# Performance work log

Measured on AMD Instinct MI355X. Metric: run time of the kernel, lower is better.

## Reference

```python
import jax, jax.numpy as jnp
import numpy as np

N = 100000
E = 1600000
D_IN = 128
HEADS = 4
C = 16  # hidden // heads
NEG_SLOPE = 0.2


def setup_inputs() -> dict:
    key = jax.random.key(0)
    ks = jax.random.split(key, 8)
    x = jax.random.normal(ks[0], (N, D_IN), dtype=jnp.float32)
    edge_index = jax.random.randint(ks[1], (2, E), 0, N, dtype=jnp.int32)
    s = 1.0 / np.sqrt(D_IN)
    W_l = jax.random.normal(ks[2], (D_IN, HEADS * C), dtype=jnp.float32) * s
    b_l = jnp.zeros((HEADS * C,), dtype=jnp.float32)
    W_r = jax.random.normal(ks[3], (D_IN, HEADS * C), dtype=jnp.float32) * s
    b_r = jnp.zeros((HEADS * C,), dtype=jnp.float32)
    att = jax.random.normal(ks[4], (HEADS, C), dtype=jnp.float32) * (1.0 / np.sqrt(C))
    bias = jnp.zeros((HEADS * C,), dtype=jnp.float32)
    W_head = jax.random.normal(ks[5], (HEADS * C, 1), dtype=jnp.float32) * (1.0 / np.sqrt(HEADS * C))
    b_head = jnp.zeros((1,), dtype=jnp.float32)
    return {"x": x, "edge_index": edge_index, "W_l": W_l, "b_l": b_l,
            "W_r": W_r, "b_r": b_r, "att": att, "bias": bias,
            "W_head": W_head, "b_head": b_head}


def reference(x, edge_index, W_l, b_l, W_r, b_r, att, bias, W_head, b_head):
    # GATv2Conv (PyG semantics, add_self_loops=True, concat=True)
    n = x.shape[0]
    # add self loops
    loops = jnp.arange(n, dtype=edge_index.dtype)
    src = jnp.concatenate([edge_index[0], loops])  # source j
    dst = jnp.concatenate([edge_index[1], loops])  # target i
    # per-node linear projections -> [N, H, C]
    x_l = (x @ W_l + b_l).reshape(n, HEADS, C)
    x_r = (x @ W_r + b_r).reshape(n, HEADS, C)
    # per-edge attention logits: att . LeakyReLU(x_l[j] + x_r[i])
    e = x_l[src] + x_r[dst]                               # [E', H, C]
    e = jnp.where(e >= 0, e, NEG_SLOPE * e)
    logits = jnp.einsum('ehc,hc->eh', e, att)             # [E', H]
    # segment softmax over incoming edges of each target node
    seg_max = jax.ops.segment_max(logits, dst, num_segments=n)  # [N, H]
    expw = jnp.exp(logits - seg_max[dst])
    seg_sum = jax.ops.segment_sum(expw, dst, num_segments=n)
    alpha = expw / seg_sum[dst]                           # [E', H]
    # weighted scatter-aggregate of source messages
    msg = alpha[:, :, None] * x_l[src]                    # [E', H, C]
    out = jax.ops.segment_sum(msg, dst, num_segments=n)   # [N, H, C]
    out = out.reshape(n, HEADS * C) + bias
    # ReLU + Linear head
    h = jax.nn.relu(out)
    return (h @ W_head + b_head).squeeze(-1)              # [N]
```

## Files before the change

### kernel.cpp

```cpp
#include <hip/hip_runtime.h>
#include <hip/hip_bf16.h>
#include <hip/hip_fp16.h>

#define HC 64
#define D_IN 128
#define NEG_SLOPE 0.2f
#define BK 64
#define BCAP2 1536
#define NBIN 2048
#define L2E 1.44269504f

using f32x4 = __attribute__((ext_vector_type(4))) float;
using f16x8 = __attribute__((ext_vector_type(8))) _Float16;
using f16x2 = __attribute__((ext_vector_type(2))) _Float16;

__global__ void k_iota(int* __restrict__ p, int n) {
    int i = blockIdx.x * blockDim.x + threadIdx.x;
    if (i < n) p[i] = i * BCAP2;
}

__global__ __launch_bounds__(256, 3) void k_proj(
    const float* __restrict__ x,
    const float* __restrict__ Wl, const float* __restrict__ bl,
    const float* __restrict__ Wr, const float* __restrict__ br,
    __half* __restrict__ xlh, float* __restrict__ xr, int N) {
    __shared__ _Float16 sWT[128 * 136];
    __shared__ _Float16 sX[32 * 136];
    const int t = threadIdx.x;
    for (int idx = t; idx < 8192; idx += 256) {
        const int k = idx >> 6;
        const int c = idx & 63;
        sWT[c * 136 + k]        = (_Float16)Wl[idx];
        sWT[(c + 64) * 136 + k] = (_Float16)Wr[idx];
    }
    const int lane = t & 63;
    const int wave = t >> 6;
    const int m = lane & 15;
    const int q = lane >> 4;
    float bfu[2];
#pragma unroll
    for (int cc = 0; cc < 2; ++cc) {
        const int ct = wave * 2 + cc;
        const int ch = (ct & 3) * 16 + m;
        bfu[cc] = (ct < 4) ? bl[ch] : br[ch];
    }
    __syncthreads();

    const int ntrip = N >> 5;
    for (int trip = blockIdx.x; trip < ntrip; trip += gridDim.x) {
        const int i0 = trip << 5;
        for (int c = t; c < 1024; c += 256) {
            const int r = c >> 5, c4 = c & 31;
            float4 v = ((const float4*)(x + (size_t)(i0 + r) * D_IN))[c4];
            _Float16* dp = &sX[r * 136 + c4 * 4];
            dp[0] = (_Float16)v.x; dp[1] = (_Float16)v.y;
            dp[2] = (_Float16)v.z; dp[3] = (_Float16)v.w;
        }
        __syncthreads();
        f16x8 af[2][4];
#pragma unroll
        for (int tt = 0; tt < 2; ++tt)
#pragma unroll
            for (int kk = 0; kk < 4; ++kk)
                af[tt][kk] = *(const f16x8*)&sX[(tt * 16 + m) * 136 + kk * 32 + q * 8];
#pragma unroll
        for (int cc = 0; cc < 2; ++cc) {
            const int ct = wave * 2 + cc;
            const _Float16* bp = &sWT[(ct * 16 + m) * 136 + q * 8];
            f32x4 acc0 = {0.f, 0.f, 0.f, 0.f};
            f32x4 acc1 = {0.f, 0.f, 0.f, 0.f};
#pragma unroll
            for (int kk = 0; kk < 4; ++kk) {
                f16x8 bf = *(const f16x8*)(bp + kk * 32);
                acc0 = __builtin_amdgcn_mfma_f32_16x16x32_f16(af[0][kk], bf, acc0, 0, 0, 0);
                acc1 = __builtin_amdgcn_mfma_f32_16x16x32_f16(af[1][kk], bf, acc1, 0, 0, 0);
            }
            const float bv = bfu[cc];
            if (ct < 4) {
                const int ch = ct * 16 + m;
#pragma unroll
                for (int r = 0; r < 4; ++r) {
                    xlh[(size_t)(i0 + q * 4 + r) * HC + ch]      = __float2half(acc0[r] + bv);
                    xlh[(size_t)(i0 + 16 + q * 4 + r) * HC + ch] = __float2half(acc1[r] + bv);
                }
            } else {
                const int ch = (ct - 4) * 16 + m;
#pragma unroll
                for (int r = 0; r < 4; ++r) {
                    xr[(size_t)(i0 + q * 4 + r) * HC + ch]      = acc0[r] + bv;
                    xr[(size_t)(i0 + 16 + q * 4 + r) * HC + ch] = acc1[r] + bv;
                }
            }
        }
        __syncthreads();
    }
}

__global__ __launch_bounds__(256) void k_scat1(const int* __restrict__ src,
                                               const int* __restrict__ dst, int E,
                                               int* __restrict__ bfill,
                                               unsigned* __restrict__ coarse) {
    __shared__ int h[NBIN], bl[NBIN], cur[NBIN];
    const int t = threadIdx.x;
    for (int i = t; i < NBIN; i += 256) { h[i] = 0; cur[i] = 0; }
    __syncthreads();
    const int beg = blockIdx.x * 4096;
    int4 d4[4], s4[4];
#pragma unroll
    for (int r = 0; r < 4; ++r) {
        const int idx = beg + 4 * t + r * 1024;
        if (idx < E) {
            d4[r] = *(const int4*)(dst + idx);
            s4[r] = *(const int4*)(src + idx);
        } else { d4[r] = make_int4(-1, -1, -1, -1); }
    }
#pragma unroll
    for (int r = 0; r < 4; ++r) {
        if (d4[r].x >= 0) {
            atomicAdd(&h[d4[r].x >> 6], 1);
            atomicAdd(&h[d4[r].y >> 6], 1);
            atomicAdd(&h[d4[r].z >> 6], 1);
            atomicAdd(&h[d4[r].w >> 6], 1);
        }
    }
    __syncthreads();
    for (int i = t; i < NBIN; i += 256)
        bl[i] = h[i] ? atomicAdd(&bfill[i], h[i]) : 0;
    __syncthreads();
#pragma unroll
    for (int r = 0; r < 4; ++r) {
        if (d4[r].x >= 0) {
            const int dd[4] = {d4[r].x, d4[r].y, d4[r].z, d4[r].w};
            const int ss[4] = {s4[r].x, s4[r].y, s4[r].z, s4[r].w};
#pragma unroll
            for (int j = 0; j < 4; ++j) {
                const int bin = dd[j] >> 6;
                const int pos = atomicAdd(&cur[bin], 1);
                coarse[bl[bin] + pos] = ((unsigned)ss[j] << 6) | (unsigned)(dd[j] & 63);
            }
        }
    }
}

__device__ __forceinline__ float redpair(float v) {
    int a = __builtin_amdgcn_update_dpp(0, __float_as_int(v), 0xB1, 0xF, 0xF, true);
    return v + __int_as_float(a);
}

__global__ __launch_bounds__(256) void k_aggs(
    const __half* __restrict__ xlh, const float* __restrict__ xr,
    const float* __restrict__ att, const float* __restrict__ bias,
    const float* __restrict__ Wh, const float* __restrict__ bh,
    const int* __restrict__ bfill, const unsigned* __restrict__ coarse,
    float* __restrict__ out, int N) {
    __shared__ int s_src[BCAP2];
    __shared__ int s_cnt[BK], s_off[BK], s_cur[BK], s_scan[BK];
    const int t = threadIdx.x;
    const int b = blockIdx.x;
    const int eb = b * BCAP2;
    const int ee = bfill[b];
    if (t < BK) { s_cnt[t] = 0; s_cur[t] = 0; }
    __syncthreads();
    unsigned er[6]; int nr = 0;
#pragma unroll
    for (int r = 0; r < 6; ++r) {
        const int idx = eb + t + r * 256;
        if (idx < ee) er[nr++] = coarse[idx];
    }
    for (int k = 0; k < nr; ++k) atomicAdd(&s_cnt[er[k] & 63], 1);
    __syncthreads();
    if (t < BK) s_scan[t] = s_cnt[t];
    __syncthreads();
    for (int o = 1; o < BK; o <<= 1) {
        int v = (t < BK && t >= o) ? s_scan[t - o] : 0;
        __syncthreads();
        if (t < BK) s_scan[t] += v;
        __syncthreads();
    }
    if (t < BK) s_off[t] = s_scan[t] - s_cnt[t];
    __syncthreads();
    for (int k = 0; k < nr; ++k) {
        const int bin = er[k] & 63;
        const int pos = atomicAdd(&s_cur[bin], 1);
        s_src[s_off[bin] + pos] = (int)(er[k] >> 6);
    }
    __syncthreads();

    const int wave = t >> 6;
    const int lane = t & 63;
    const int sub  = lane & 7;
    const int slot = lane >> 3;
    const _Float16* xlhp = (const _Float16*)xlh;

    const float4 atA = *(const float4*)(att + 8 * sub);
    const float4 atB = *(const float4*)(att + 8 * sub + 4);
    f16x2 at[4];
    at[0][0] = (_Float16)(atA.x * L2E); at[0][1] = (_Float16)(atA.y * L2E);
    at[1][0] = (_Float16)(atA.z * L2E); at[1][1] = (_Float16)(atA.w * L2E);
    at[2][0] = (_Float16)(atB.x * L2E); at[2][1] = (_Float16)(atB.y * L2E);
    at[3][0] = (_Float16)(atB.z * L2E); at[3][1] = (_Float16)(atB.w * L2E);
    const f16x2 c02 = {(_Float16)NEG_SLOPE, (_Float16)NEG_SLOPE};
    const float4 biA = *(const float4*)(bias + 8 * sub);
    const float4 biB = *(const float4*)(bias + 8 * sub + 4);
    const float4 whA = *(const float4*)(Wh + 8 * sub);
    const float4 whB = *(const float4*)(Wh + 8 * sub + 4);
    const float bhv = bh[0];

    for (int k16 = 0; k16 < 16; ++k16) {
        const int nl = wave + 4 * k16;
        const int i = (b << 6) + nl;
        if (i >= N) continue;
        const int beg = s_off[nl];
        const int cnt = s_cnt[nl];

        const float4 xrA = *(const float4*)(xr + ((size_t)i << 6) + 8 * sub);
        const float4 xrB = *(const float4*)(xr + ((size_t)i << 6) + 8 * sub + 4);
        f16x2 xri[4];
        xri[0][0] = (_Float16)xrA.x; xri[0][1] = (_Float16)xrA.y;
        xri[1][0] = (_Float16)xrA.z; xri[1][1] = (_Float16)xrA.w;
        xri[2][0] = (_Float16)xrB.x; xri[2][1] = (_Float16)xrB.y;
        xri[3][0] = (_Float16)xrB.z; xri[3][1] = (_Float16)xrB.w;
        const uint4 xliraw = *(const uint4*)(xlhp + ((size_t)i << 6) + 8 * sub);
        f16x2 xli[4];
        xli[0] = __builtin_bit_cast(f16x2, xliraw.x);
        xli[1] = __builtin_bit_cast(f16x2, xliraw.y);
        xli[2] = __builtin_bit_cast(f16x2, xliraw.z);
        xli[3] = __builtin_bit_cast(f16x2, xliraw.w);

        float t0 = 0.f;
#pragma unroll
        for (int c = 0; c < 4; ++c) {
            f16x2 w = xli[c] + xri[c];
            w = __builtin_elementwise_max(w, w * c02);
            t0 = __builtin_amdgcn_fdot2(at[c], w, t0, false);
        }
        t0 = redpair(t0);
        const float pe0 = (slot == 0) ? exp2f(t0) : 0.f;
        float s = pe0;
        float a[8];
#pragma unroll
        for (int c = 0; c < 4; ++c) {
            a[2 * c]     = pe0 * (float)xli[c][0];
            a[2 * c + 1] = pe0 * (float)xli[c][1];
        }

        int p = 0;
#define EDGE_GROUP(JEXPR, PRED)                                              \
    {                                                                        \
        const int jj = (JEXPR);                                              \
        const uint4 raw = *(const uint4*)(xlhp + ((size_t)jj << 6) + 8 * sub);\
        f16x2 xv[4];                                                         \
        xv[0] = __builtin_bit_cast(f16x2, raw.x);                            \
        xv[1] = __builtin_bit_cast(f16x2, raw.y);                            \
        xv[2] = __builtin_bit_cast(f16x2, raw.z);                            \
        xv[3] = __builtin_bit_cast(f16x2, raw.w);                            \
        float tt = 0.f;                                                      \
        _Pragma("unroll")                                                    \
        for (int c = 0; c < 4; ++c) {                                        \
            f16x2 w = xv[c] + xri[c];                                        \
            w = __builtin_elementwise_max(w, w * c02);                       \
            tt = __builtin_amdgcn_fdot2(at[c], w, tt, false);                \
        }                                                                    \
        tt = redpair(tt);                                                    \
        const float pe = (PRED) ? exp2f(tt) : 0.f;                           \
        s += pe;                                                             \
        _Pragma("unroll")                                                    \
        for (int c = 0; c < 4; ++c) {                                        \
            a[2 * c]     = fmaf(pe, (float)xv[c][0], a[2 * c]);              \
            a[2 * c + 1] = fmaf(pe, (float)xv[c][1], a[2 * c + 1]);          \
        }                                                                    \
    }
        for (; p + 16 <= cnt; p += 16) {
            const int j0 = s_src[beg + p + slot];
            const int j1 = s_src[beg + p + 8 + slot];
            EDGE_GROUP(j0, true)
            EDGE_GROUP(j1, true)
        }
        if (p + 8 <= cnt) {
            const int j0 = s_src[beg + p + slot];
            EDGE_GROUP(j0, true)
            p += 8;
        }
        const int rem = cnt - p;
        if (rem > 0) {
            const int idx = p + slot;
            const int j0 = s_src[beg + ((idx < cnt) ? idx : (cnt - 1))];
            EDGE_GROUP(j0, slot < rem)
        }
#undef EDGE_GROUP

        s += __shfl_xor(s, 8);  s += __shfl_xor(s, 16);  s += __shfl_xor(s, 32);
#pragma unroll
        for (int c = 0; c < 8; ++c) {
            a[c] += __shfl_xor(a[c], 8);
            a[c] += __shfl_xor(a[c], 16);
            a[c] += __shfl_xor(a[c], 32);
        }
        const float inv = 1.f / s;
        float y = fmaxf(a[0] * inv + biA.x, 0.f) * whA.x
                + fmaxf(a[1] * inv + biA.y, 0.f) * whA.y
                + fmaxf(a[2] * inv + biA.z, 0.f) * whA.z
                + fmaxf(a[3] * inv + biA.w, 0.f) * whA.w
                + fmaxf(a[4] * inv + biB.x, 0.f) * whB.x
                + fmaxf(a[5] * inv + biB.y, 0.f) * whB.y
                + fmaxf(a[6] * inv + biB.z, 0.f) * whB.z
                + fmaxf(a[7] * inv + biB.w, 0.f) * whB.w;
        y += __shfl_xor(y, 1);
        y += __shfl_xor(y, 2);
        y += __shfl_xor(y, 4);
        if (lane == 0) out[i] = y + bhv;
    }
}

extern "C" void kernel_launch(void* const* d_in, const int* in_sizes, int n_in,
                              void* d_out, int out_size, void* d_ws, size_t ws_size,
                              hipStream_t stream) {
    const float* x   = (const float*)d_in[0];
    const int*   ei  = (const int*)d_in[1];
    const float* Wl  = (const float*)d_in[2];
    const float* bl  = (const float*)d_in[3];
    const float* Wr  = (const float*)d_in[4];
    const float* br  = (const float*)d_in[5];
    const float* att = (const float*)d_in[6];
    const float* bias= (const float*)d_in[7];
    const float* Wh  = (const float*)d_in[8];
    const float* bh  = (const float*)d_in[9];
    float* out = (float*)d_out;

    const int N = in_sizes[0] / D_IN;
    const int E = in_sizes[1] / 2;
    const int* src = ei;
    const int* dst = ei + E;
    const int nbkt = (N + BK - 1) / BK;

    auto align = [](size_t v) { return (v + 255) & ~(size_t)255; };
    char* ws = (char*)d_ws;
    size_t off = 0;
    __half* xlh     = (__half*)(ws + off);   off = align(off + (size_t)N * HC * 2);
    float* xr       = (float*)(ws + off);    off = align(off + (size_t)N * HC * 4);
    int*   bfill    = (int*)(ws + off);      off = align(off + NBIN * 4);
    unsigned* coarse= (unsigned*)(ws + off); off = align(off + (size_t)NBIN * BCAP2 * 4);
    (void)ws_size;

    k_iota<<<8, 256, 0, stream>>>(bfill, NBIN);

    k_proj<<<1024, 256, 0, stream>>>(x, Wl, bl, Wr, br, xlh, xr, N);

    k_scat1<<<(E + 4095) / 4096, 256, 0, stream>>>(src, dst, E, bfill, coarse);

    k_aggs<<<nbkt, 256, 0, stream>>>(xlh, xr, att, bias, Wh, bh,
                                     bfill, coarse, out, N);
}
```

Baseline: 216.6 us.

## Shrink scatter blocks, double aggregation block size, and hoist edge gather loads

The scatter kernel now handles 1024 edges per block instead of 4096. It reuses the histogram array as the cursor, which frees shared memory and launches four times as many blocks. The aggregation kernel moves to 512-thread blocks, so 8 waves each handle 8 destination nodes, with launch bounds asking for higher occupancy. The edge loop now splits loads from compute so two gathers are in flight before the math, and the tail handles up to 16 leftover edges in one pass. This aims at more latency hiding on the gather-bound aggregation, at the cost of more global atomics on the bin counters in the scatter.

Result: slower. 283.5 us (+30.9%).

```diff
diff --git a/kernel.cpp b/kernel.cpp
--- a/kernel.cpp
+++ b/kernel.cpp
@@ -100,44 +100,40 @@
                                                const int* __restrict__ dst, int E,
                                                int* __restrict__ bfill,
                                                unsigned* __restrict__ coarse) {
-    __shared__ int h[NBIN], bl[NBIN], cur[NBIN];
+    __shared__ int h[NBIN], bl[NBIN];
     const int t = threadIdx.x;
-    for (int i = t; i < NBIN; i += 256) { h[i] = 0; cur[i] = 0; }
-    __syncthreads();
-    const int beg = blockIdx.x * 4096;
-    int4 d4[4], s4[4];
-#pragma unroll
-    for (int r = 0; r < 4; ++r) {
-        const int idx = beg + 4 * t + r * 1024;
-        if (idx < E) {
-            d4[r] = *(const int4*)(dst + idx);
-            s4[r] = *(const int4*)(src + idx);
-        } else { d4[r] = make_int4(-1, -1, -1, -1); }
-    }
-#pragma unroll
-    for (int r = 0; r < 4; ++r) {
-        if (d4[r].x >= 0) {
-            atomicAdd(&h[d4[r].x >> 6], 1);
-            atomicAdd(&h[d4[r].y >> 6], 1);
-            atomicAdd(&h[d4[r].z >> 6], 1);
-            atomicAdd(&h[d4[r].w >> 6], 1);
-        }
-    }
-    __syncthreads();
-    for (int i = t; i < NBIN; i += 256)
-        bl[i] = h[i] ? atomicAdd(&bfill[i], h[i]) : 0;
-    __syncthreads();
-#pragma unroll
-    for (int r = 0; r < 4; ++r) {
-        if (d4[r].x >= 0) {
-            const int dd[4] = {d4[r].x, d4[r].y, d4[r].z, d4[r].w};
-            const int ss[4] = {s4[r].x, s4[r].y, s4[r].z, s4[r].w};
-#pragma unroll
-            for (int j = 0; j < 4; ++j) {
-                const int bin = dd[j] >> 6;
-                const int pos = atomicAdd(&cur[bin], 1);
-                coarse[bl[bin] + pos] = ((unsigned)ss[j] << 6) | (unsigned)(dd[j] & 63);
-            }
+    for (int i = t; i < NBIN; i += 256) h[i] = 0;
+    __syncthreads();
+    const int idx = blockIdx.x * 1024 + 4 * t;
+    int4 d4, s4;
+    if (idx < E) {
+        d4 = *(const int4*)(dst + idx);
+        s4 = *(const int4*)(src + idx);
+    } else {
+        d4 = make_int4(-1, -1, -1, -1);
+        s4 = make_int4(0, 0, 0, 0);
+    }
+    if (d4.x >= 0) {
+        atomicAdd(&h[d4.x >> 6], 1);
+        atomicAdd(&h[d4.y >> 6], 1);
+        atomicAdd(&h[d4.z >> 6], 1);
+        atomicAdd(&h[d4.w >> 6], 1);
+    }
+    __syncthreads();
+    for (int i = t; i < NBIN; i += 256) {
+        const int hv = h[i];
+        bl[i] = hv ? atomicAdd(&bfill[i], hv) : 0;
+        h[i] = 0;
+    }
+    __syncthreads();
+    if (d4.x >= 0) {
+        const int dd[4] = {d4.x, d4.y, d4.z, d4.w};
+        const int ss[4] = {s4.x, s4.y, s4.z, s4.w};
+#pragma unroll
+        for (int j = 0; j < 4; ++j) {
+            const int bin = dd[j] >> 6;
+            const int pos = atomicAdd(&h[bin], 1);
+            coarse[bl[bin] + pos] = ((unsigned)ss[j] << 6) | (unsigned)(dd[j] & 63);
         }
     }
 }
@@ -147,7 +143,7 @@
     return v + __int_as_float(a);
 }
 
-__global__ __launch_bounds__(256) void k_aggs(
+__global__ __launch_bounds__(512, 8) void k_aggs(
     const __half* __restrict__ xlh, const float* __restrict__ xr,
     const float* __restrict__ att, const float* __restrict__ bias,
     const float* __restrict__ Wh, const float* __restrict__ bh,
@@ -161,10 +157,10 @@
     const int ee = bfill[b];
     if (t < BK) { s_cnt[t] = 0; s_cur[t] = 0; }
     __syncthreads();
-    unsigned er[6]; int nr = 0;
-#pragma unroll
-    for (int r = 0; r < 6; ++r) {
-        const int idx = eb + t + r * 256;
+    unsigned er[3]; int nr = 0;
+#pragma unroll
+    for (int r = 0; r < 3; ++r) {
+        const int idx = eb + t + r * 512;
         if (idx < ee) er[nr++] = coarse[idx];
     }
     for (int k = 0; k < nr; ++k) atomicAdd(&s_cnt[er[k] & 63], 1);
@@ -206,54 +202,16 @@
     const float4 whB = *(const float4*)(Wh + 8 * sub + 4);
     const float bhv = bh[0];
 
-    for (int k16 = 0; k16 < 16; ++k16) {
-        const int nl = wave + 4 * k16;
-        const int i = (b << 6) + nl;
-        if (i >= N) continue;
-        const int beg = s_off[nl];
-        const int cnt = s_cnt[nl];
-
-        const float4 xrA = *(const float4*)(xr + ((size_t)i << 6) + 8 * sub);
-        const float4 xrB = *(const float4*)(xr + ((size_t)i << 6) + 8 * sub + 4);
-        f16x2 xri[4];
-        xri[0][0] = (_Float16)xrA.x; xri[0][1] = (_Float16)xrA.y;
-        xri[1][0] = (_Float16)xrA.z; xri[1][1] = (_Float16)xrA.w;
-        xri[2][0] = (_Float16)xrB.x; xri[2][1] = (_Float16)xrB.y;
-        xri[3][0] = (_Float16)xrB.z; xri[3][1] = (_Float16)xrB.w;
-        const uint4 xliraw = *(const uint4*)(xlhp + ((size_t)i << 6) + 8 * sub);
-        f16x2 xli[4];
-        xli[0] = __builtin_bit_cast(f16x2, xliraw.x);
-        xli[1] = __builtin_bit_cast(f16x2, xliraw.y);
-        xli[2] = __builtin_bit_cast(f16x2, xliraw.z);
-        xli[3] = __builtin_bit_cast(f16x2, xliraw.w);
-
-        float t0 = 0.f;
-#pragma unroll
-        for (int c = 0; c < 4; ++c) {
-            f16x2 w = xli[c] + xri[c];
-            w = __builtin_elementwise_max(w, w * c02);
-            t0 = __builtin_amdgcn_fdot2(at[c], w, t0, false);
-        }
-        t0 = redpair(t0);
-        const float pe0 = (slot == 0) ? exp2f(t0) : 0.f;
-        float s = pe0;
-        float a[8];
-#pragma unroll
-        for (int c = 0; c < 4; ++c) {
-            a[2 * c]     = pe0 * (float)xli[c][0];
-            a[2 * c + 1] = pe0 * (float)xli[c][1];
-        }
-
-        int p = 0;
-#define EDGE_GROUP(JEXPR, PRED)                                              \
+#define EG_LOAD(RAW, J)                                                      \
+    const uint4 RAW = *(const uint4*)(xlhp + ((size_t)(J) << 6) + 8 * sub);
+
+#define EG_COMP(RAW, PRED)                                                   \
     {                                                                        \
-        const int jj = (JEXPR);                                              \
-        const uint4 raw = *(const uint4*)(xlhp + ((size_t)jj << 6) + 8 * sub);\
         f16x2 xv[4];                                                         \
-        xv[0] = __builtin_bit_cast(f16x2, raw.x);                            \
-        xv[1] = __builtin_bit_cast(f16x2, raw.y);                            \
-        xv[2] = __builtin_bit_cast(f16x2, raw.z);                            \
-        xv[3] = __builtin_bit_cast(f16x2, raw.w);                            \
+        xv[0] = __builtin_bit_cast(f16x2, RAW.x);                            \
+        xv[1] = __builtin_bit_cast(f16x2, RAW.y);                            \
+        xv[2] = __builtin_bit_cast(f16x2, RAW.z);                            \
+        xv[3] = __builtin_bit_cast(f16x2, RAW.w);                            \
         float tt = 0.f;                                                      \
         _Pragma("unroll")                                                    \
         for (int c = 0; c < 4; ++c) {                                        \
@@ -270,24 +228,71 @@
             a[2 * c + 1] = fmaf(pe, (float)xv[c][1], a[2 * c + 1]);          \
         }                                                                    \
     }
+
+    for (int k16 = 0; k16 < 8; ++k16) {
+        const int nl = wave + 8 * k16;
+        const int i = (b << 6) + nl;
+        if (i >= N) continue;
+        const int beg = s_off[nl];
+        const int cnt = s_cnt[nl];
+
+        const float4 xrA = *(const float4*)(xr + ((size_t)i << 6) + 8 * sub);
+        const float4 xrB = *(const float4*)(xr + ((size_t)i << 6) + 8 * sub + 4);
+        f16x2 xri[4];
+        xri[0][0] = (_Float16)xrA.x; xri[0][1] = (_Float16)xrA.y;
+        xri[1][0] = (_Float16)xrA.z; xri[1][1] = (_Float16)xrA.w;
+        xri[2][0] = (_Float16)xrB.x; xri[2][1] = (_Float16)xrB.y;
+        xri[3][0] = (_Float16)xrB.z; xri[3][1] = (_Float16)xrB.w;
+        const uint4 xliraw = *(const uint4*)(xlhp + ((size_t)i << 6) + 8 * sub);
+        f16x2 xli[4];
+        xli[0] = __builtin_bit_cast(f16x2, xliraw.x);
+        xli[1] = __builtin_bit_cast(f16x2, xliraw.y);
+        xli[2] = __builtin_bit_cast(f16x2, xliraw.z);
+        xli[3] = __builtin_bit_cast(f16x2, xliraw.w);
+
+        float t0 = 0.f;
+#pragma unroll
+        for (int c = 0; c < 4; ++c) {
+            f16x2 w = xli[c] + xri[c];
+            w = __builtin_elementwise_max(w, w * c02);
+            t0 = __builtin_amdgcn_fdot2(at[c], w, t0, false);
+        }
+        t0 = redpair(t0);
+        const float pe0 = (slot == 0) ? exp2f(t0) : 0.f;
+        float s = pe0;
+        float a[8];
+#pragma unroll
+        for (int c = 0; c < 4; ++c) {
+            a[2 * c]     = pe0 * (float)xli[c][0];
+            a[2 * c + 1] = pe0 * (float)xli[c][1];
+        }
+
+        int p = 0;
         for (; p + 16 <= cnt; p += 16) {
             const int j0 = s_src[beg + p + slot];
             const int j1 = s_src[beg + p + 8 + slot];
-            EDGE_GROUP(j0, true)
-            EDGE_GROUP(j1, true)
-        }
-        if (p + 8 <= cnt) {
-            const int j0 = s_src[beg + p + slot];
-            EDGE_GROUP(j0, true)
-            p += 8;
+            EG_LOAD(raw0, j0)
+            EG_LOAD(raw1, j1)
+            EG_COMP(raw0, true)
+            EG_COMP(raw1, true)
         }
         const int rem = cnt - p;
         if (rem > 0) {
-            const int idx = p + slot;
-            const int j0 = s_src[beg + ((idx < cnt) ? idx : (cnt - 1))];
-            EDGE_GROUP(j0, slot < rem)
-        }
-#undef EDGE_GROUP
+            const int iA = p + slot;
+            const int jA = s_src[beg + ((iA < cnt) ? iA : (cnt - 1))];
+            EG_LOAD(rawA, jA)
+            if (rem > 8) {
+                const int iB = p + 8 + slot;
+                const int jB = s_src[beg + ((iB < cnt) ? iB : (cnt - 1))];
+                EG_LOAD(rawB, jB)
+                EG_COMP(rawA, true)
+                EG_COMP(rawB, iB < cnt)
+            } else {
+                EG_COMP(rawA, iA < cnt)
+            }
+        }
+#undef EG_LOAD
+#undef EG_COMP
 
         s += __shfl_xor(s, 8);  s += __shfl_xor(s, 16);  s += __shfl_xor(s, 32);
 #pragma unroll
@@ -346,8 +351,8 @@
 
     k_proj<<<1024, 256, 0, stream>>>(x, Wl, bl, Wr, br, xlh, xr, N);
 
-    k_scat1<<<(E + 4095) / 4096, 256, 0, stream>>>(src, dst, E, bfill, coarse);
-
-    k_aggs<<<nbkt, 256, 0, stream>>>(xlh, xr, att, bias, Wh, bh,
+    k_scat1<<<(E + 1023) / 1024, 256, 0, stream>>>(src, dst, E, bfill, coarse);
+
+    k_aggs<<<nbkt, 512, 0, stream>>>(xlh, xr, att, bias, Wh, bh,
                                      bfill, coarse, out, N);
 }
```

## Keep projection weights in registers, load x directly, fold iota into k_proj

Applied to the files above, without the earlier changes.

The projection kernel stops staging W and x through shared memory. Each wave now keeps its weight fragments in registers, and each lane loads its x slice from global memory and converts it to fp16, which removes the LDS traffic and the per-tile __syncthreads. The separate iota launch is merged into the first blocks of k_proj, saving one kernel launch, and the occupancy hint is raised to 4. In exchange, x reads are now strided per lane, which may coalesce less well, and weight loads happen per block from global memory.

Result: no change. 220.3 us (+1.7%).

```diff
diff --git a/kernel.cpp b/kernel.cpp
--- a/kernel.cpp
+++ b/kernel.cpp
@@ -14,66 +14,69 @@
 using f16x8 = __attribute__((ext_vector_type(8))) _Float16;
 using f16x2 = __attribute__((ext_vector_type(2))) _Float16;
 
-__global__ void k_iota(int* __restrict__ p, int n) {
-    int i = blockIdx.x * blockDim.x + threadIdx.x;
-    if (i < n) p[i] = i * BCAP2;
-}
-
-__global__ __launch_bounds__(256, 3) void k_proj(
+__global__ __launch_bounds__(256, 4) void k_proj(
     const float* __restrict__ x,
     const float* __restrict__ Wl, const float* __restrict__ bl,
     const float* __restrict__ Wr, const float* __restrict__ br,
-    __half* __restrict__ xlh, float* __restrict__ xr, int N) {
-    __shared__ _Float16 sWT[128 * 136];
-    __shared__ _Float16 sX[32 * 136];
+    __half* __restrict__ xlh, float* __restrict__ xr,
+    int* __restrict__ bfill, int N) {
+    if (blockIdx.x < 8) {
+        const int i = blockIdx.x * 256 + threadIdx.x;
+        bfill[i] = i * BCAP2;
+    }
     const int t = threadIdx.x;
-    for (int idx = t; idx < 8192; idx += 256) {
-        const int k = idx >> 6;
-        const int c = idx & 63;
-        sWT[c * 136 + k]        = (_Float16)Wl[idx];
-        sWT[(c + 64) * 136 + k] = (_Float16)Wr[idx];
-    }
     const int lane = t & 63;
     const int wave = t >> 6;
     const int m = lane & 15;
     const int q = lane >> 4;
+
+    f16x8 bf[2][4];
     float bfu[2];
 #pragma unroll
     for (int cc = 0; cc < 2; ++cc) {
         const int ct = wave * 2 + cc;
         const int ch = (ct & 3) * 16 + m;
+        const float* W = (ct < 4) ? Wl : Wr;
         bfu[cc] = (ct < 4) ? bl[ch] : br[ch];
-    }
-    __syncthreads();
+#pragma unroll
+        for (int kk = 0; kk < 4; ++kk) {
+            const float* wp = W + (size_t)(kk * 32 + q * 8) * 64 + ch;
+            f16x8 v;
+#pragma unroll
+            for (int e = 0; e < 8; ++e)
+                v[e] = (_Float16)wp[(size_t)e * 64];
+            bf[cc][kk] = v;
+        }
+    }
 
     const int ntrip = N >> 5;
     for (int trip = blockIdx.x; trip < ntrip; trip += gridDim.x) {
         const int i0 = trip << 5;
-        for (int c = t; c < 1024; c += 256) {
-            const int r = c >> 5, c4 = c & 31;
-            float4 v = ((const float4*)(x + (size_t)(i0 + r) * D_IN))[c4];
-            _Float16* dp = &sX[r * 136 + c4 * 4];
-            dp[0] = (_Float16)v.x; dp[1] = (_Float16)v.y;
-            dp[2] = (_Float16)v.z; dp[3] = (_Float16)v.w;
-        }
-        __syncthreads();
         f16x8 af[2][4];
 #pragma unroll
-        for (int tt = 0; tt < 2; ++tt)
-#pragma unroll
-            for (int kk = 0; kk < 4; ++kk)
-                af[tt][kk] = *(const f16x8*)&sX[(tt * 16 + m) * 136 + kk * 32 + q * 8];
+        for (int tt = 0; tt < 2; ++tt) {
+            const float* xp = x + (size_t)(i0 + tt * 16 + m) * D_IN + q * 8;
+#pragma unroll
+            for (int kk = 0; kk < 4; ++kk) {
+                const float4 f0 = *(const float4*)(xp + kk * 32);
+                const float4 f1 = *(const float4*)(xp + kk * 32 + 4);
+                f16x8 v;
+                v[0] = (_Float16)f0.x; v[1] = (_Float16)f0.y;
+                v[2] = (_Float16)f0.z; v[3] = (_Float16)f0.w;
+                v[4] = (_Float16)f1.x; v[5] = (_Float16)f1.y;
+                v[6] = (_Float16)f1.z; v[7] = (_Float16)f1.w;
+                af[tt][kk] = v;
+            }
+        }
 #pragma unroll
         for (int cc = 0; cc < 2; ++cc) {
             const int ct = wave * 2 + cc;
-            const _Float16* bp = &sWT[(ct * 16 + m) * 136 + q * 8];
             f32x4 acc0 = {0.f, 0.f, 0.f, 0.f};
             f32x4 acc1 = {0.f, 0.f, 0.f, 0.f};
 #pragma unroll
             for (int kk = 0; kk < 4; ++kk) {
-                f16x8 bf = *(const f16x8*)(bp + kk * 32);
-                acc0 = __builtin_amdgcn_mfma_f32_16x16x32_f16(af[0][kk], bf, acc0, 0, 0, 0);
-                acc1 = __builtin_amdgcn_mfma_f32_16x16x32_f16(af[1][kk], bf, acc1, 0, 0, 0);
+                acc0 = __builtin_amdgcn_mfma_f32_16x16x32_f16(af[0][kk], bf[cc][kk], acc0, 0, 0, 0);
+                acc1 = __builtin_amdgcn_mfma_f32_16x16x32_f16(af[1][kk], bf[cc][kk], acc1, 0, 0, 0);
             }
             const float bv = bfu[cc];
             if (ct < 4) {
@@ -92,7 +95,6 @@
                 }
             }
         }
-        __syncthreads();
     }
 }
 
@@ -342,9 +344,7 @@
     unsigned* coarse= (unsigned*)(ws + off); off = align(off + (size_t)NBIN * BCAP2 * 4);
     (void)ws_size;
 
-    k_iota<<<8, 256, 0, stream>>>(bfill, NBIN);
-
-    k_proj<<<1024, 256, 0, stream>>>(x, Wl, bl, Wr, br, xlh, xr, N);
+    k_proj<<<1024, 256, 0, stream>>>(x, Wl, bl, Wr, br, xlh, xr, bfill, N);
 
     k_scat1<<<(E + 4095) / 4096, 256, 0, stream>>>(src, dst, E, bfill, coarse);
 
```

## Split each aggregation bucket across two blocks and use fp16 dot2 accumulation

Applied to the files above, without the earlier changes.

Each 64-node bucket is now handled by two blocks, each filtering the bucket's edges down to its 32-node half, which doubles the grid to improve occupancy and load balance. The per-edge weighted accumulation converts the exponentiated weight to fp16 and uses fdot2 with masked pairs instead of fp32 conversions plus FMAs. A DPP row-shift add replaces the first cross-lane shuffle in the reductions. In exchange, the coarse edge list is read twice, and the attention weights are rounded to fp16, which reduces precision and can overflow fp16 when logits are large.

Measured after the change: 209.4 us. 3.3% less time.

```diff
diff --git a/kernel.cpp b/kernel.cpp
--- a/kernel.cpp
+++ b/kernel.cpp
@@ -6,6 +6,7 @@
 #define D_IN 128
 #define NEG_SLOPE 0.2f
 #define BK 64
+#define BKH 32
 #define BCAP2 1536
 #define NBIN 2048
 #define L2E 1.44269504f
@@ -146,6 +147,10 @@
     int a = __builtin_amdgcn_update_dpp(0, __float_as_int(v), 0xB1, 0xF, 0xF, true);
     return v + __int_as_float(a);
 }
+__device__ __forceinline__ float red8(float v) {
+    int a = __builtin_amdgcn_update_dpp(0, __float_as_int(v), 0x128, 0xF, 0xF, true);
+    return v + __int_as_float(a);
+}
 
 __global__ __launch_bounds__(256) void k_aggs(
     const __half* __restrict__ xlh, const float* __restrict__ xr,
@@ -154,33 +159,37 @@
     const int* __restrict__ bfill, const unsigned* __restrict__ coarse,
     float* __restrict__ out, int N) {
     __shared__ int s_src[BCAP2];
-    __shared__ int s_cnt[BK], s_off[BK], s_cur[BK], s_scan[BK];
+    __shared__ int s_cnt[BKH], s_off[BKH], s_cur[BKH], s_scan[BKH];
     const int t = threadIdx.x;
-    const int b = blockIdx.x;
-    const int eb = b * BCAP2;
-    const int ee = bfill[b];
-    if (t < BK) { s_cnt[t] = 0; s_cur[t] = 0; }
+    const int bkt = blockIdx.x >> 1;
+    const int half = blockIdx.x & 1;
+    const int eb = bkt * BCAP2;
+    const int ee = bfill[bkt];
+    if (t < BKH) { s_cnt[t] = 0; s_cur[t] = 0; }
     __syncthreads();
     unsigned er[6]; int nr = 0;
 #pragma unroll
     for (int r = 0; r < 6; ++r) {
         const int idx = eb + t + r * 256;
-        if (idx < ee) er[nr++] = coarse[idx];
-    }
-    for (int k = 0; k < nr; ++k) atomicAdd(&s_cnt[er[k] & 63], 1);
-    __syncthreads();
-    if (t < BK) s_scan[t] = s_cnt[t];
-    __syncthreads();
-    for (int o = 1; o < BK; o <<= 1) {
-        int v = (t < BK && t >= o) ? s_scan[t - o] : 0;
+        if (idx < ee) {
+            const unsigned e = coarse[idx];
+            if (((e >> 5) & 1u) == (unsigned)half) er[nr++] = e;
+        }
+    }
+    for (int k = 0; k < nr; ++k) atomicAdd(&s_cnt[er[k] & 31], 1);
+    __syncthreads();
+    if (t < BKH) s_scan[t] = s_cnt[t];
+    __syncthreads();
+    for (int o = 1; o < BKH; o <<= 1) {
+        int v = (t < BKH && t >= o) ? s_scan[t - o] : 0;
         __syncthreads();
-        if (t < BK) s_scan[t] += v;
+        if (t < BKH) s_scan[t] += v;
         __syncthreads();
     }
-    if (t < BK) s_off[t] = s_scan[t] - s_cnt[t];
+    if (t < BKH) s_off[t] = s_scan[t] - s_cnt[t];
     __syncthreads();
     for (int k = 0; k < nr; ++k) {
-        const int bin = er[k] & 63;
+        const int bin = er[k] & 31;
         const int pos = atomicAdd(&s_cur[bin], 1);
         s_src[s_off[bin] + pos] = (int)(er[k] >> 6);
     }
@@ -200,15 +209,16 @@
     at[2][0] = (_Float16)(atB.x * L2E); at[2][1] = (_Float16)(atB.y * L2E);
     at[3][0] = (_Float16)(atB.z * L2E); at[3][1] = (_Float16)(atB.w * L2E);
     const f16x2 c02 = {(_Float16)NEG_SLOPE, (_Float16)NEG_SLOPE};
+    const _Float16 h0 = (_Float16)0.f;
     const float4 biA = *(const float4*)(bias + 8 * sub);
     const float4 biB = *(const float4*)(bias + 8 * sub + 4);
     const float4 whA = *(const float4*)(Wh + 8 * sub);
     const float4 whB = *(const float4*)(Wh + 8 * sub + 4);
     const float bhv = bh[0];
 
-    for (int k16 = 0; k16 < 16; ++k16) {
-        const int nl = wave + 4 * k16;
-        const int i = (b << 6) + nl;
+    for (int k8 = 0; k8 < 8; ++k8) {
+        const int nl = wave + 4 * k8;
+        const int i = bkt * 64 + half * 32 + nl;
         if (i >= N) continue;
         const int beg = s_off[nl];
         const int cnt = s_cnt[nl];
@@ -235,13 +245,15 @@
             t0 = __builtin_amdgcn_fdot2(at[c], w, t0, false);
         }
         t0 = redpair(t0);
-        const float pe0 = (slot == 0) ? exp2f(t0) : 0.f;
-        float s = pe0;
+        const _Float16 pe0h = (slot == 0) ? (_Float16)exp2f(t0) : h0;
+        const f16x2 p0A = {pe0h, h0};
+        const f16x2 p0B = {h0, pe0h};
+        float s = (float)pe0h;
         float a[8];
 #pragma unroll
         for (int c = 0; c < 4; ++c) {
-            a[2 * c]     = pe0 * (float)xli[c][0];
-            a[2 * c + 1] = pe0 * (float)xli[c][1];
+            a[2 * c]     = __builtin_amdgcn_fdot2(xli[c], p0A, 0.f, false);
+            a[2 * c + 1] = __builtin_amdgcn_fdot2(xli[c], p0B, 0.f, false);
         }
 
         int p = 0;
@@ -262,12 +274,14 @@
             tt = __builtin_amdgcn_fdot2(at[c], w, tt, false);                \
         }                                                                    \
         tt = redpair(tt);                                                    \
-        const float pe = (PRED) ? exp2f(tt) : 0.f;                           \
-        s += pe;                                                             \
+        const _Float16 peh = (PRED) ? (_Float16)exp2f(tt) : h0;              \
+        const f16x2 pA = {peh, h0};                                          \
+        const f16x2 pB = {h0, peh};                                          \
+        s += (float)peh;                                                     \
         _Pragma("unroll")                                                    \
         for (int c = 0; c < 4; ++c) {                                        \
-            a[2 * c]     = fmaf(pe, (float)xv[c][0], a[2 * c]);              \
-            a[2 * c + 1] = fmaf(pe, (float)xv[c][1], a[2 * c + 1]);          \
+            a[2 * c]     = __builtin_amdgcn_fdot2(xv[c], pA, a[2 * c], false);\
+            a[2 * c + 1] = __builtin_amdgcn_fdot2(xv[c], pB, a[2 * c + 1], false);\
         }                                                                    \
     }
         for (; p + 16 <= cnt; p += 16) {
@@ -289,10 +303,10 @@
         }
 #undef EDGE_GROUP
 
-        s += __shfl_xor(s, 8);  s += __shfl_xor(s, 16);  s += __shfl_xor(s, 32);
+        s = red8(s);  s += __shfl_xor(s, 16);  s += __shfl_xor(s, 32);
 #pragma unroll
         for (int c = 0; c < 8; ++c) {
-            a[c] += __shfl_xor(a[c], 8);
+            a[c] = red8(a[c]);
             a[c] += __shfl_xor(a[c], 16);
             a[c] += __shfl_xor(a[c], 32);
         }
@@ -348,6 +362,6 @@
 
     k_scat1<<<(E + 4095) / 4096, 256, 0, stream>>>(src, dst, E, bfill, coarse);
 
-    k_aggs<<<nbkt, 256, 0, stream>>>(xlh, xr, att, bias, Wh, bh,
-                                     bfill, coarse, out, N);
-}
+    k_aggs<<<nbkt * 2, 256, 0, stream>>>(xlh, xr, att, bias, Wh, bh,
+                                         bfill, coarse, out, N);
+}
```
